# Kernel tuning notes

Measured on AMD Instinct MI355X. Metric: run time of the kernel, lower is better.

Reference implementation:

```python
import jax, jax.numpy as jnp
import numpy as np

K = 2  # top-k experts per token


def setup_inputs() -> dict:
    key = jax.random.key(0)
    k1, k2, k3, k4 = jax.random.split(key, 4)
    B, S, D, E = 4, 4096, 1024, 64
    x = jax.random.normal(k1, (B, S, D), dtype=jnp.float32)
    gate_w = jax.random.normal(k2, (E, D), dtype=jnp.float32) * (1.0 / np.sqrt(D))
    noise_weight = jax.random.normal(k3, (E,), dtype=jnp.float32) * 0.02
    noise = jax.random.normal(k4, (B, S, E), dtype=jnp.float32)  # randn_like(logits) * noisy_std(=1.0)
    return {"x": x, "gate_w": gate_w, "noise_weight": noise_weight, "noise": noise}


def reference(x, gate_w, noise_weight, noise):
    E = gate_w.shape[0]
    # logits = x @ W^T  -> [B, S, E]
    logits = jnp.einsum("bsd,ed->bse", x, gate_w)
    logits_noisy = logits + noise * noise_weight  # noisy_std = 1.0 folded into `noise`
    top_vals, top_idx = jax.lax.top_k(logits_noisy, K)  # [B,S,K]
    # scatter top-k logits into a -inf mask, then softmax over experts
    keep = jax.nn.one_hot(top_idx, E, dtype=jnp.bool_).any(axis=-2)  # [B,S,E]
    neg_inf = jnp.finfo(logits_noisy.dtype).min
    sparse = jnp.where(keep, logits_noisy, neg_inf)
    weights = jax.nn.softmax(sparse, axis=-1)
    return weights, top_idx
```

## Files before the change

kernel.cpp:

```cpp
#include <hip/hip_runtime.h>
#include <math.h>


#define DDIM 1024
#define NEXP 64
#define NTOK 16384
#define CPW 4
#define CHUNK_SH 12288

typedef float f4 __attribute__((ext_vector_type(4)));
typedef short s8 __attribute__((ext_vector_type(8)));
typedef unsigned int u32;

static __device__ __forceinline__ void split3(float f, short& h, short& m, short& l) {
    const u32 uf = __float_as_uint(f);
    h = (short)(uf >> 16);
    const float r1 = f - __uint_as_float(uf & 0xffff0000u);
    const u32 u1 = __float_as_uint(r1);
    m = (short)(u1 >> 16);
    const float r2 = r1 - __uint_as_float(u1 & 0xffff0000u);
    l = (short)(__float_as_uint(r2) >> 16);
}

__global__ __launch_bounds__(256)
void w_prep(const float* __restrict__ gw, short* __restrict__ wimg) {
    const int uid = blockIdx.x * 256 + threadIdx.x;
    const int c   = uid >> 9;
    const int kk  = (uid >> 8) & 1;
    const int e   = (uid >> 2) & 63;
    const int q   = uid & 3;
    const int k0  = c * 64 + kk * 32 + q * 8;
    const float* src = gw + (size_t)e * DDIM + k0;
    s8 hv, mv, lv;
    #pragma unroll
    for (int j = 0; j < 8; ++j) {
        short h, m, l;
        split3(src[j], h, m, l);
        hv[j] = h; mv[j] = m; lv[j] = l;
    }
    const size_t base = (size_t)c * 1536 + (kk * 3) * 256
                      + (e >> 4) * 64 + q * 16 + (e & 15);
    *(s8*)(wimg + (base      ) * 8) = hv;
    *(s8*)(wimg + (base + 256) * 8) = mv;
    *(s8*)(wimg + (base + 512) * 8) = lv;
}

static __device__ __forceinline__ bool bt(float av, int ai, float bv, int bi) {
    return av > bv || (av == bv && ai < bi);
}

__global__ __launch_bounds__(256, 3)
void moe_fused(const float* __restrict__ x,
               const short* __restrict__ wimg,
               const float* __restrict__ nwt,
               const float* __restrict__ noise,
               float* __restrict__ out_w,
               float* __restrict__ out_i)
{
    __shared__ float red[4][16][NEXP];

    const int tid  = threadIdx.x;
    const int lane = tid & 63;
    const int wv   = tid >> 6;
    const int m    = lane & 15;
    const int q    = lane >> 4;
    const int tokBase = blockIdx.x * 16;

    const float* xrow = x + (size_t)(tokBase + m) * DDIM + wv * (CPW * 64) + q * 8;

    f4 acc0[4], acc1[4];
    #pragma unroll
    for (int t = 0; t < 4; ++t) { acc0[t] = (f4)0.f; acc1[t] = (f4)0.f; }

    f4 As[4];
    As[0] = *(const f4*)(xrow);
    As[1] = *(const f4*)(xrow + 4);
    As[2] = *(const f4*)(xrow + 32);
    As[3] = *(const f4*)(xrow + 36);

    #pragma unroll
    for (int cc = 0; cc < CPW; ++cc) {
        const short* cb = wimg + (size_t)(wv * CPW + cc) * CHUNK_SH;

        s8 ah[2], am[2], al[2];
        const float* sv = (const float*)&As[0];
        #pragma unroll
        for (int kk = 0; kk < 2; ++kk)
            #pragma unroll
            for (int j = 0; j < 8; ++j) {
                short h, mm, l;
                split3(sv[kk * 8 + j], h, mm, l);
                ah[kk][j] = h; am[kk][j] = mm; al[kk][j] = l;
            }

        if (cc + 1 < CPW) {
            const float* s = xrow + (cc + 1) * 64;
            As[0] = *(const f4*)(s);
            As[1] = *(const f4*)(s + 4);
            As[2] = *(const f4*)(s + 32);
            As[3] = *(const f4*)(s + 36);
        }

        #pragma unroll
        for (int kk = 0; kk < 2; ++kk) {
            s8 bh[4], bm[4], bl[4];
            #pragma unroll
            for (int t = 0; t < 4; ++t) {
                const int pb = (kk * 3) * 256 + t * 64 + lane;
                bh[t] = *(const s8*)(cb + (size_t)(pb      ) * 8);
                bm[t] = *(const s8*)(cb + (size_t)(pb + 256) * 8);
                bl[t] = *(const s8*)(cb + (size_t)(pb + 512) * 8);
            }
            #pragma unroll
            for (int t = 0; t < 4; ++t) {
                acc0[t] = __builtin_amdgcn_mfma_f32_16x16x32_bf16(ah[kk], bh[t], acc0[t], 0, 0, 0);
                acc1[t] = __builtin_amdgcn_mfma_f32_16x16x32_bf16(ah[kk], bm[t], acc1[t], 0, 0, 0);
                acc1[t] = __builtin_amdgcn_mfma_f32_16x16x32_bf16(am[kk], bh[t], acc1[t], 0, 0, 0);
                acc1[t] = __builtin_amdgcn_mfma_f32_16x16x32_bf16(ah[kk], bl[t], acc1[t], 0, 0, 0);
                acc1[t] = __builtin_amdgcn_mfma_f32_16x16x32_bf16(am[kk], bm[t], acc1[t], 0, 0, 0);
                acc1[t] = __builtin_amdgcn_mfma_f32_16x16x32_bf16(al[kk], bh[t], acc1[t], 0, 0, 0);
            }
        }
    }

    #pragma unroll
    for (int t = 0; t < 4; ++t)
        #pragma unroll
        for (int r = 0; r < 4; ++r)
            red[wv][q * 4 + r][m + 16 * t] = acc0[t][r] + acc1[t][r];

    __syncthreads();

    const float nw = nwt[lane];
    #pragma unroll
    for (int r = 0; r < 4; ++r) {
        const int lt  = wv * 4 + r;
        const int tok = tokBase + lt;
        const float sum = (red[0][lt][lane] + red[1][lt][lane])
                        + (red[2][lt][lane] + red[3][lt][lane]);
        const float ln = fmaf(noise[(size_t)tok * NEXP + lane], nw, sum);

        float v1 = ln; int i1 = lane;
        #pragma unroll
        for (int off = 32; off > 0; off >>= 1) {
            const float vo = __shfl_xor(v1, off, 64);
            const int   io = __shfl_xor(i1, off, 64);
            if (bt(vo, io, v1, i1)) { v1 = vo; i1 = io; }
        }
        float v2 = (lane == i1) ? -3.4e38f : ln; int i2 = lane;
        #pragma unroll
        for (int off = 32; off > 0; off >>= 1) {
            const float vo = __shfl_xor(v2, off, 64);
            const int   io = __shfl_xor(i2, off, 64);
            if (bt(vo, io, v2, i2)) { v2 = vo; i2 = io; }
        }

        const float d   = expf(v2 - v1);
        const float inv = 1.f / (1.f + d);
        const float wgt = (lane == i1) ? inv : ((lane == i2) ? d * inv : 0.f);
        out_w[(size_t)tok * NEXP + lane] = wgt;
        if (lane == 0) {
            out_i[(size_t)tok * 2]     = (float)i1;
            out_i[(size_t)tok * 2 + 1] = (float)i2;
        }
    }
}

extern "C" void kernel_launch(void* const* d_in, const int* in_sizes, int n_in,
                              void* d_out, int out_size, void* d_ws, size_t ws_size,
                              hipStream_t stream) {
    const float* x     = (const float*)d_in[0];
    const float* gw    = (const float*)d_in[1];
    const float* nwt   = (const float*)d_in[2];
    const float* noise = (const float*)d_in[3];
    float* out_w = (float*)d_out;
    float* out_i = (float*)d_out + (size_t)NTOK * NEXP;
    short* wimg  = (short*)d_ws;

    hipLaunchKernelGGL(w_prep, dim3(32), dim3(256), 0, stream, gw, wimg);
    hipLaunchKernelGGL(moe_fused, dim3(NTOK / 16), dim3(256), 0, stream,
                       x, wimg, nwt, noise, out_w, out_i);
}
```

Before: 125.1 us.

## Split K across eight waves per block and interleave B loads with MFMAs

Doubles the block to 512 threads so each 16-token tile splits the 1024-long reduction over eight waves with two chunks each, rather than four waves with four chunks. The LDS reduction and softmax epilogue now sum eight partials, and each wave handles two tokens. B fragment loads are moved inline next to their MFMAs to cut register pressure, and launch bounds request higher occupancy. This adds parallelism and latency hiding in exchange for a larger shared-memory reduction and a longer block-wide sync.

```diff
diff --git a/kernel.cpp b/kernel.cpp
--- a/kernel.cpp
+++ b/kernel.cpp
@@ -5,7 +5,8 @@
 #define DDIM 1024
 #define NEXP 64
 #define NTOK 16384
-#define CPW 4
+#define WPB 8
+#define CPW 2
 #define CHUNK_SH 12288
 
 typedef float f4 __attribute__((ext_vector_type(4)));
@@ -49,7 +50,7 @@
     return av > bv || (av == bv && ai < bi);
 }
 
-__global__ __launch_bounds__(256, 3)
+__global__ __launch_bounds__(512, 8)
 void moe_fused(const float* __restrict__ x,
                const short* __restrict__ wimg,
                const float* __restrict__ nwt,
@@ -57,7 +58,7 @@
                float* __restrict__ out_w,
                float* __restrict__ out_i)
 {
-    __shared__ float red[4][16][NEXP];
+    __shared__ float red[WPB][16][NEXP];
 
     const int tid  = threadIdx.x;
     const int lane = tid & 63;
@@ -103,22 +104,18 @@
 
         #pragma unroll
         for (int kk = 0; kk < 2; ++kk) {
-            s8 bh[4], bm[4], bl[4];
             #pragma unroll
             for (int t = 0; t < 4; ++t) {
                 const int pb = (kk * 3) * 256 + t * 64 + lane;
-                bh[t] = *(const s8*)(cb + (size_t)(pb      ) * 8);
-                bm[t] = *(const s8*)(cb + (size_t)(pb + 256) * 8);
-                bl[t] = *(const s8*)(cb + (size_t)(pb + 512) * 8);
-            }
-            #pragma unroll
-            for (int t = 0; t < 4; ++t) {
-                acc0[t] = __builtin_amdgcn_mfma_f32_16x16x32_bf16(ah[kk], bh[t], acc0[t], 0, 0, 0);
-                acc1[t] = __builtin_amdgcn_mfma_f32_16x16x32_bf16(ah[kk], bm[t], acc1[t], 0, 0, 0);
-                acc1[t] = __builtin_amdgcn_mfma_f32_16x16x32_bf16(am[kk], bh[t], acc1[t], 0, 0, 0);
-                acc1[t] = __builtin_amdgcn_mfma_f32_16x16x32_bf16(ah[kk], bl[t], acc1[t], 0, 0, 0);
-                acc1[t] = __builtin_amdgcn_mfma_f32_16x16x32_bf16(am[kk], bm[t], acc1[t], 0, 0, 0);
-                acc1[t] = __builtin_amdgcn_mfma_f32_16x16x32_bf16(al[kk], bh[t], acc1[t], 0, 0, 0);
+                const s8 bh = *(const s8*)(cb + (size_t)(pb      ) * 8);
+                const s8 bm = *(const s8*)(cb + (size_t)(pb + 256) * 8);
+                const s8 bl = *(const s8*)(cb + (size_t)(pb + 512) * 8);
+                acc0[t] = __builtin_amdgcn_mfma_f32_16x16x32_bf16(ah[kk], bh, acc0[t], 0, 0, 0);
+                acc1[t] = __builtin_amdgcn_mfma_f32_16x16x32_bf16(ah[kk], bm, acc1[t], 0, 0, 0);
+                acc1[t] = __builtin_amdgcn_mfma_f32_16x16x32_bf16(am[kk], bh, acc1[t], 0, 0, 0);
+                acc1[t] = __builtin_amdgcn_mfma_f32_16x16x32_bf16(ah[kk], bl, acc1[t], 0, 0, 0);
+                acc1[t] = __builtin_amdgcn_mfma_f32_16x16x32_bf16(am[kk], bm, acc1[t], 0, 0, 0);
+                acc1[t] = __builtin_amdgcn_mfma_f32_16x16x32_bf16(al[kk], bh, acc1[t], 0, 0, 0);
             }
         }
     }
@@ -133,11 +130,13 @@
 
     const float nw = nwt[lane];
     #pragma unroll
-    for (int r = 0; r < 4; ++r) {
-        const int lt  = wv * 4 + r;
+    for (int r = 0; r < 2; ++r) {
+        const int lt  = wv * 2 + r;
         const int tok = tokBase + lt;
-        const float sum = (red[0][lt][lane] + red[1][lt][lane])
-                        + (red[2][lt][lane] + red[3][lt][lane]);
+        const float sum = ((red[0][lt][lane] + red[1][lt][lane])
+                         + (red[2][lt][lane] + red[3][lt][lane]))
+                        + ((red[4][lt][lane] + red[5][lt][lane])
+                         + (red[6][lt][lane] + red[7][lt][lane]));
         const float ln = fmaf(noise[(size_t)tok * NEXP + lane], nw, sum);
 
         float v1 = ln; int i1 = lane;
@@ -178,6 +177,6 @@
     short* wimg  = (short*)d_ws;
 
     hipLaunchKernelGGL(w_prep, dim3(32), dim3(256), 0, stream, gw, wimg);
-    hipLaunchKernelGGL(moe_fused, dim3(NTOK / 16), dim3(256), 0, stream,
+    hipLaunchKernelGGL(moe_fused, dim3(NTOK / 16), dim3(512), 0, stream,
                        x, wimg, nwt, noise, out_w, out_i);
 }
```

After: 201.3 us. 1.61x slower.
